# Kernel tuning notes

Measured on AMD Instinct MI355X. Metric: run time of the kernel, lower is better.

Reference implementation:

```python
import jax, jax.numpy as jnp
import numpy as np

DIM = 2048
N_HEADS = 16
KV_LORA = 512
NOPE = 128
ROPE = 64
V_DIM = 128
QK_DIM = NOPE + ROPE  # 192
B, S = 2, 2048
ROPE_THETA = 10000.0
ROPE_FACTOR = 40.0
BETA_FAST, BETA_SLOW = 32, 1
ORIG_LEN, MAX_LEN = 4096, 16384
MSCALE_ARG = 1.0
EPS = 1e-6


def _precompute_freqs(seqlen):
    # DeepSeek YaRN-corrected rotary frequencies (interleaved-pair convention).
    d = ROPE
    freqs = 1.0 / (ROPE_THETA ** (np.arange(0, d, 2, dtype=np.float64) / d))
    if MAX_LEN > ORIG_LEN:
        def corr_dim(n_rot):
            return d * np.log(ORIG_LEN / (n_rot * 2 * np.pi)) / (2 * np.log(ROPE_THETA))
        low = max(int(np.floor(corr_dim(BETA_FAST))), 0)
        high = min(int(np.ceil(corr_dim(BETA_SLOW))), d - 1)
        smooth = 1.0 - np.clip((np.arange(d // 2) - low) / max(high - low, 1e-3), 0, 1)
        freqs = freqs / ROPE_FACTOR * (1 - smooth) + freqs * smooth
    t = np.arange(seqlen, dtype=np.float64)
    ang = np.outer(t, freqs)  # [S, d/2]
    return np.cos(ang).astype(np.float32), np.sin(ang).astype(np.float32)


def softmax_scale():
    scale = QK_DIM ** -0.5
    if MAX_LEN > ORIG_LEN:
        m = 0.1 * MSCALE_ARG * float(np.log(ROPE_FACTOR)) + 1.0
        scale = scale * m * m
    return scale


def setup_inputs() -> dict:
    key = jax.random.key(0)
    ks = jax.random.split(key, 6)
    w_std = 0.02
    fc, fs = _precompute_freqs(S)
    return {
        "x": jax.random.normal(ks[0], (B, S, DIM), jnp.float32),
        "wq": jax.random.normal(ks[1], (N_HEADS * QK_DIM, DIM), jnp.float32) * w_std,
        "wkv_a": jax.random.normal(ks[2], (KV_LORA + ROPE, DIM), jnp.float32) * w_std,
        "kv_norm_w": jnp.ones((KV_LORA,), jnp.float32),
        "wkv_b": jax.random.normal(ks[3], (N_HEADS * (NOPE + V_DIM), KV_LORA), jnp.float32) * w_std,
        "wo": jax.random.normal(ks[4], (DIM, N_HEADS * V_DIM), jnp.float32) * w_std,
        "freqs_cos": jnp.asarray(fc),
        "freqs_sin": jnp.asarray(fs),
    }


def _apply_rotary(x, cos, sin):
    # x: [B, S, H, d]; interleaved complex pairs, cos/sin: [S, d/2]
    xr = x.reshape(*x.shape[:-1], -1, 2)
    x_re, x_im = xr[..., 0], xr[..., 1]
    c = cos[None, :, None, :]
    s = sin[None, :, None, :]
    y_re = x_re * c - x_im * s
    y_im = x_re * s + x_im * c
    return jnp.stack((y_re, y_im), axis=-1).reshape(x.shape)


def _rmsnorm(x, w):
    return x * jax.lax.rsqrt(jnp.mean(x * x, axis=-1, keepdims=True) + EPS) * w


def reference(x, wq, wkv_a, kv_norm_w, wkv_b, wo, freqs_cos, freqs_sin):
    b, s, _ = x.shape
    # Q projection (q_lora_rank == 0 path)
    q = (x @ wq.T).reshape(b, s, N_HEADS, QK_DIM)
    q_nope, q_pe = q[..., :NOPE], q[..., NOPE:]
    q_pe = _apply_rotary(q_pe, freqs_cos, freqs_sin)
    # Low-rank KV compression
    kv = x @ wkv_a.T  # [B, S, 512+64]
    kv_c, k_pe = kv[..., :KV_LORA], kv[..., KV_LORA:]
    k_pe = _apply_rotary(k_pe[:, :, None, :], freqs_cos, freqs_sin)  # [B,S,1,64]
    kv_c = _rmsnorm(kv_c, kv_norm_w)
    kvb = (kv_c @ wkv_b.T).reshape(b, s, N_HEADS, NOPE + V_DIM)
    k_nope, v = kvb[..., :NOPE], kvb[..., NOPE:]
    k = jnp.concatenate([k_nope, jnp.broadcast_to(k_pe, (b, s, N_HEADS, ROPE))], axis=-1)
    # Causal attention
    scores = jnp.einsum("bshd,bthd->bhst", q, k) * softmax_scale()
    causal = jnp.tril(jnp.ones((s, s), bool))
    scores = jnp.where(causal[None, None], scores, jnp.float32(-1e30))
    p = jax.nn.softmax(scores, axis=-1)
    out = jnp.einsum("bhst,bthd->bshd", p, v).reshape(b, s, N_HEADS * V_DIM)
    return out @ wo.T
```

## Files before the change

### kernel.cpp

```cpp
#include <hip/hip_runtime.h>
#include <math.h>

#define NH      16
#define D_NOPE  128
#define D_ROPE  64
#define D_QK    192
#define D_V     128
#define KV_LORA 512
#define NB      2
#define SEQ     2048
#define NTOK    (NB*SEQ)
#define QROW    (NH*D_QK)
#define KVBROW  (NH*(D_NOPE+D_V))
#define EPSF    1e-6f

typedef unsigned short u16;
typedef float  floatx4 __attribute__((ext_vector_type(4)));
typedef __bf16 bf16x8  __attribute__((ext_vector_type(8)));
typedef u16    u16x4   __attribute__((ext_vector_type(4)));
typedef u16    u16x8   __attribute__((ext_vector_type(8)));

__device__ __forceinline__ u16 f2bf(float f) {
    unsigned u = __builtin_bit_cast(unsigned, f);
    return (u16)((u + 0x7fffu + ((u >> 16) & 1u)) >> 16);
}

__device__ __forceinline__ void async_copy16(const void* g, void* l) {
    __builtin_amdgcn_global_load_lds(
        (const __attribute__((address_space(1))) unsigned int*)g,
        (__attribute__((address_space(3))) unsigned int*)l,
        16, 0, 0);
}

__global__ __launch_bounds__(256) void cast_all(const float* __restrict__ x,
                                                const float* __restrict__ wq,
                                                const float* __restrict__ wkva,
                                                const float* __restrict__ wkvb,
                                                const float* __restrict__ wo,
                                                u16* __restrict__ xb,
                                                u16* __restrict__ wqb,
                                                u16* __restrict__ wkvab,
                                                u16* __restrict__ wkvbb,
                                                u16* __restrict__ wob) {
    int blk = blockIdx.x;
    const float* src; u16* dst; bool pad = false;
    if (blk < 8192)        { src = x;    dst = xb; }
    else if (blk < 14336)  { blk -= 8192;  src = wq;   dst = wqb; }
    else if (blk < 15616)  { blk -= 14336; src = wkva; dst = wkvab; pad = true; }
    else if (blk < 17664)  { blk -= 15616; src = wkvb; dst = wkvbb; }
    else                   { blk -= 17664; src = wo;   dst = wob; }
    const int i = (blk * 256 + threadIdx.x) * 4;
    u16x4 o;
    if (pad && (i >> 11) >= 576) {
        o[0] = 0; o[1] = 0; o[2] = 0; o[3] = 0;
    } else {
        const float4 v = *(const float4*)&src[i];
        o[0] = f2bf(v.x); o[1] = f2bf(v.y); o[2] = f2bf(v.z); o[3] = f2bf(v.w);
    }
    *(u16x4*)&dst[i] = o;
}

template<int MODE>
__global__ __launch_bounds__(256) void gemm_mfma(const u16* __restrict__ A,
                                                 const u16* __restrict__ B,
                                                 void* __restrict__ Cout,
                                                 u16* __restrict__ kbuf,
                                                 u16* __restrict__ vT,
                                                 int M, int N, int K) {
    __shared__ u16 As[128 * 32];
    __shared__ u16 Bs[128 * 32];
    const int tid  = threadIdx.x;
    const int wave = tid >> 6, lane = tid & 63;
    const int m0 = blockIdx.y * 128, n0 = blockIdx.x * 128;
    const int wm = (wave & 1) * 64, wn = (wave >> 1) * 64;

    const int srow = wave * 32 + (lane >> 2);
    const int kch  = (lane & 3) * 8;
    const u16* gA0 = A + (size_t)(m0 + srow) * K + kch;
    const u16* gA1 = gA0 + (size_t)16 * K;
    const u16* gB0 = B + (size_t)(n0 + srow) * K + kch;
    const u16* gB1 = gB0 + (size_t)16 * K;
    u16* lA0 = &As[(wave * 32) * 32];
    u16* lA1 = &As[(wave * 32 + 16) * 32];
    u16* lB0 = &Bs[(wave * 32) * 32];
    u16* lB1 = &Bs[(wave * 32 + 16) * 32];

    floatx4 acc[4][4];
#pragma unroll
    for (int i = 0; i < 4; ++i)
#pragma unroll
        for (int j = 0; j < 4; ++j) acc[i][j] = 0.f;

    const int lrow = lane & 15;
    const int lkh  = (lane >> 4) * 8;

    for (int k0 = 0; k0 < K; k0 += 32) {
        __syncthreads();
        async_copy16(gA0 + k0, lA0);
        async_copy16(gA1 + k0, lA1);
        async_copy16(gB0 + k0, lB0);
        async_copy16(gB1 + k0, lB1);
        __syncthreads();
        bf16x8 a[4], b[4];
#pragma unroll
        for (int mi = 0; mi < 4; ++mi)
            a[mi] = *(const bf16x8*)&As[(wm + mi * 16 + lrow) * 32 + lkh];
#pragma unroll
        for (int ni = 0; ni < 4; ++ni)
            b[ni] = *(const bf16x8*)&Bs[(wn + ni * 16 + lrow) * 32 + lkh];
#pragma unroll
        for (int mi = 0; mi < 4; ++mi)
#pragma unroll
            for (int ni = 0; ni < 4; ++ni)
                acc[mi][ni] = __builtin_amdgcn_mfma_f32_16x16x32_bf16(
                    a[mi], b[ni], acc[mi][ni], 0, 0, 0);
    }

    const int crow = (lane >> 4) * 4, ccol = lane & 15;
#pragma unroll
    for (int mi = 0; mi < 4; ++mi)
#pragma unroll
        for (int ni = 0; ni < 4; ++ni) {
            const int m = m0 + wm + mi * 16 + crow;
            const int c = n0 + wn + ni * 16 + ccol;
            if (MODE == 0) {
                float* cp = (float*)Cout + (size_t)m * N + c;
#pragma unroll
                for (int r = 0; r < 4; ++r) cp[(size_t)r * N] = acc[mi][ni][r];
            } else if (MODE == 1) {
                u16* cp = (u16*)Cout + (size_t)m * N + c;
#pragma unroll
                for (int r = 0; r < 4; ++r) cp[(size_t)r * N] = f2bf(acc[mi][ni][r]);
            } else {
                const int hh = c >> 8, j = c & 255;
                const int bb = m >> 11, t = m & 2047;
                if (j < 128) {
#pragma unroll
                    for (int r = 0; r < 4; ++r)
                        kbuf[(((size_t)hh * 2 + bb) * 2048 + t + r) * 192 + j] =
                            f2bf(acc[mi][ni][r]);
                } else {
                    u16x4 pk;
#pragma unroll
                    for (int r = 0; r < 4; ++r) pk[r] = f2bf(acc[mi][ni][r]);
                    *(u16x4*)&vT[(((size_t)hh * 2 + bb) * 128 + (j - 128)) * 2048 + t] = pk;
                }
            }
        }
}


__global__ __launch_bounds__(256) void kv_fix(const float* __restrict__ kv_raw,
                                              const float* __restrict__ w,
                                              const float* __restrict__ fcos,
                                              const float* __restrict__ fsin,
                                              u16* __restrict__ kvn_bf,
                                              u16* __restrict__ kbuf) {
    const int row = blockIdx.x;
    const int tid = threadIdx.x;
    const float* src = kv_raw + (size_t)row * 640;
    const float v0 = src[tid];
    const float v1 = src[256 + tid];
    float ss = v0 * v0 + v1 * v1;
#pragma unroll
    for (int off = 32; off > 0; off >>= 1) ss += __shfl_down(ss, off, 64);
    __shared__ float red[4];
    __shared__ float kpe_s[64];
    if ((tid & 63) == 0) red[tid >> 6] = ss;
    if (tid < 32) {
        const int s = row & (SEQ - 1);
        const float c  = fcos[s * 32 + tid];
        const float sn = fsin[s * 32 + tid];
        const float xr = src[KV_LORA + 2 * tid];
        const float xi = src[KV_LORA + 2 * tid + 1];
        kpe_s[2 * tid]     = xr * c - xi * sn;
        kpe_s[2 * tid + 1] = xr * sn + xi * c;
    }
    __syncthreads();
    const float tot = red[0] + red[1] + red[2] + red[3];
    const float inv = rsqrtf(tot * (1.0f / KV_LORA) + EPSF);
    kvn_bf[(size_t)row * KV_LORA + tid]       = f2bf(v0 * inv * w[tid]);
    kvn_bf[(size_t)row * KV_LORA + 256 + tid] = f2bf(v1 * inv * w[256 + tid]);
    const int bb = row >> 11, t = row & 2047;
    const int hh = tid >> 4, dg = (tid & 15) * 4;
    u16x4 pk;
#pragma unroll
    for (int j = 0; j < 4; ++j) pk[j] = f2bf(kpe_s[dg + j]);
    *(u16x4*)&kbuf[(((size_t)hh * 2 + bb) * 2048 + t) * 192 + 128 + dg] = pk;
}

__global__ __launch_bounds__(256, 2) void attn_mfma(const u16* __restrict__ qbf,
                                                    const u16* __restrict__ kbuf,
                                                    const u16* __restrict__ vT,
                                                    u16* __restrict__ att,
                                                    float scale) {
    __shared__ __attribute__((aligned(16))) u16 Ks[2][6 * 64 * 32];
    __shared__ __attribute__((aligned(16))) u16 Ps[4][32 * 72];
    const int x = blockIdx.x;
    const int qt_base = (x & 1) ? (15 - (x >> 1)) : (x >> 1);
    const int qt = blockIdx.z ? (15 - qt_base) : qt_base;
    const int h = blockIdx.y, b = blockIdx.z;
    const int tid = threadIdx.x, wave = tid >> 6, lane = tid & 63;
    const int l15 = lane & 15, lg = lane >> 4;

    const u16* kb_base = kbuf + ((size_t)(h * 2 + b)) * 2048 * 192;
    const u16* vt_base = vT   + ((size_t)(h * 2 + b)) * 128 * 2048;

    int qrow[2];
    bf16x8 qf[2][6];
#pragma unroll
    for (int g = 0; g < 2; ++g) {
        qrow[g] = qt * 128 + g * 64 + wave * 16 + l15;
        const size_t qoff = ((size_t)(b * SEQ + qrow[g])) * QROW + h * 192 + lg * 8;
#pragma unroll
        for (int s = 0; s < 6; ++s) qf[g][s] = *(const bf16x8*)&qbf[qoff + s * 32];
    }

    floatx4 oacc[2][8];
#pragma unroll
    for (int g = 0; g < 2; ++g)
#pragma unroll
        for (int v = 0; v < 8; ++v) oacc[g][v] = 0.f;
    float m_run[2] = {-1e30f, -1e30f}, l_run[2] = {0.f, 0.f};

    auto stageK = [&](int bufi, int tt) {
#pragma unroll
        for (int i = 0; i < 6; ++i) {
            const int base = (wave * 6 + i) * 64;
            const int slot = base + lane;
            const int s = slot >> 8, r = slot & 255, tk = r >> 2, ch = r & 3;
            async_copy16(kb_base + ((size_t)(tt + tk)) * 192 + s * 32 + ch * 8,
                         &Ks[bufi][base * 8]);
        }
    };

    const int kt_max = 2 * qt + 1;
    stageK(0, 0);
    __syncthreads();

    for (int kt = 0; kt <= kt_max; ++kt) {
        const int t0 = kt * 64;
        const int cur = kt & 1;

        const u16* vrow = vt_base + (size_t)l15 * 2048 + t0 + lg * 8;
        bf16x8 vregA[8], vregB[8];
#pragma unroll
        for (int vt = 0; vt < 8; ++vt)
            vregA[vt] = *(const bf16x8*)&vrow[(size_t)vt * 16 * 2048];

        if (kt < kt_max) stageK(cur ^ 1, t0 + 64);

        floatx4 sacc[2][4];
#pragma unroll
        for (int g = 0; g < 2; ++g)
#pragma unroll
            for (int mt = 0; mt < 4; ++mt) sacc[g][mt] = 0.f;
        __builtin_amdgcn_s_setprio(1);
#pragma unroll
        for (int s = 0; s < 6; ++s) {
#pragma unroll
            for (int mt = 0; mt < 4; ++mt) {
                const bf16x8 kf = *(const bf16x8*)&Ks[cur][(s * 64 + mt * 16 + l15) * 32 + lg * 8];
#pragma unroll
                for (int g = 0; g < 2; ++g)
                    sacc[g][mt] = __builtin_amdgcn_mfma_f32_16x16x32_bf16(
                        kf, qf[g][s], sacc[g][mt], 0, 0, 0);
            }
        }
        __builtin_amdgcn_s_setprio(0);

#pragma unroll
        for (int vt = 0; vt < 8; ++vt)
            vregB[vt] = *(const bf16x8*)&vrow[(size_t)vt * 16 * 2048 + 32];

        float alpha[2];
#pragma unroll
        for (int g = 0; g < 2; ++g) {
            const bool full = (t0 + 63) <= (qt * 128 + g * 64 + wave * 16);
            float p[16];
            float tmax = -1e30f;
#pragma unroll
            for (int mt = 0; mt < 4; ++mt)
#pragma unroll
                for (int r = 0; r < 4; ++r) {
                    float v = sacc[g][mt][r] * scale;
                    if (!full) {
                        const int tglob = t0 + mt * 16 + lg * 4 + r;
                        v = (tglob <= qrow[g]) ? v : -1e30f;
                    }
                    p[mt * 4 + r] = v;
                    tmax = fmaxf(tmax, v);
                }
            tmax = fmaxf(tmax, __shfl_xor(tmax, 16));
            tmax = fmaxf(tmax, __shfl_xor(tmax, 32));
            const float mnew = fmaxf(m_run[g], tmax);
            alpha[g] = __expf(m_run[g] - mnew);
            m_run[g] = mnew;
            float rsum = 0.f;
#pragma unroll
            for (int k = 0; k < 16; ++k) { p[k] = __expf(p[k] - mnew); rsum += p[k]; }
            rsum += __shfl_xor(rsum, 16);
            rsum += __shfl_xor(rsum, 32);
            l_run[g] = l_run[g] * alpha[g] + rsum;
#pragma unroll
            for (int mt = 0; mt < 4; ++mt) {
                u16x4 pk;
#pragma unroll
                for (int r = 0; r < 4; ++r) pk[r] = f2bf(p[mt * 4 + r]);
                *(u16x4*)&Ps[wave][(g * 16 + l15) * 72 + mt * 16 + lg * 4] = pk;
            }
        }
#pragma unroll
        for (int g = 0; g < 2; ++g) {
            float af[4];
#pragma unroll
            for (int r = 0; r < 4; ++r) af[r] = __shfl(alpha[g], lg * 4 + r);
#pragma unroll
            for (int vt = 0; vt < 8; ++vt)
#pragma unroll
                for (int r = 0; r < 4; ++r) oacc[g][vt][r] *= af[r];
        }
        __builtin_amdgcn_s_setprio(1);
#pragma unroll
        for (int s = 0; s < 2; ++s) {
            bf16x8 pf[2];
#pragma unroll
            for (int g = 0; g < 2; ++g)
                pf[g] = *(const bf16x8*)&Ps[wave][(g * 16 + l15) * 72 + s * 32 + lg * 8];
#pragma unroll
            for (int vt = 0; vt < 8; ++vt) {
                const bf16x8 vf = s ? vregB[vt] : vregA[vt];
#pragma unroll
                for (int g = 0; g < 2; ++g)
                    oacc[g][vt] = __builtin_amdgcn_mfma_f32_16x16x32_bf16(
                        pf[g], vf, oacc[g][vt], 0, 0, 0);
            }
        }
        __builtin_amdgcn_s_setprio(0);

        __syncthreads();
    }
#pragma unroll
    for (int g = 0; g < 2; ++g) {
        float lf[4];
#pragma unroll
        for (int r = 0; r < 4; ++r) lf[r] = 1.0f / __shfl(l_run[g], lg * 4 + r);
#pragma unroll
        for (int vt = 0; vt < 8; ++vt)
#pragma unroll
            for (int r = 0; r < 4; ++r) {
                const int orow = b * SEQ + qt * 128 + g * 64 + wave * 16 + lg * 4 + r;
                att[(size_t)orow * 2048 + h * 128 + vt * 16 + l15] =
                    f2bf(oacc[g][vt][r] * lf[r]);
            }
    }
}

extern "C" void kernel_launch(void* const* d_in, const int* in_sizes, int n_in,
                              void* d_out, int out_size, void* d_ws, size_t ws_size,
                              hipStream_t stream) {
    const float* x     = (const float*)d_in[0];
    const float* wq    = (const float*)d_in[1];
    const float* wkv_a = (const float*)d_in[2];
    const float* knw   = (const float*)d_in[3];
    const float* wkv_b = (const float*)d_in[4];
    const float* wo    = (const float*)d_in[5];
    const float* fcos  = (const float*)d_in[6];
    const float* fsin  = (const float*)d_in[7];
    float* out = (float*)d_out;

    char* w = (char*)d_ws;
    u16*   x_bf    = (u16*)w;  w += (size_t)NTOK * 2048 * 2;
    u16*   wq_bf   = (u16*)w;  w += (size_t)QROW * 2048 * 2;
    u16*   wkva_bf = (u16*)w;  w += (size_t)640 * 2048 * 2;
    u16*   wkvb_bf = (u16*)w;  w += (size_t)KVBROW * KV_LORA * 2;
    u16*   wo_bf   = (u16*)w;  w += (size_t)2048 * 2048 * 2;
    u16*   q_bf    = (u16*)w;  w += (size_t)NTOK * QROW * 2;
    float* kv_raw  = (float*)w; w += (size_t)NTOK * 640 * 4;
    u16*   kvn_bf  = (u16*)w;  w += (size_t)NTOK * KV_LORA * 2;
    u16*   kbuf    = (u16*)w;  w += (size_t)NH * NB * SEQ * 192 * 2;
    u16*   vT      = (u16*)w;  w += (size_t)NH * NB * 128 * SEQ * 2;
    u16*   att_bf  = (u16*)w;  w += (size_t)NTOK * 2048 * 2;

    const double mm = 0.1 * 1.0 * log(40.0) + 1.0;
    const float scale = (float)((1.0 / sqrt((double)D_QK)) * mm * mm);

    dim3 blk(256);
    cast_all<<<dim3(21760), blk, 0, stream>>>(x, wq, wkv_a, wkv_b, wo,
                                              x_bf, wq_bf, wkva_bf, wkvb_bf, wo_bf);
    gemm_mfma<1><<<dim3(QROW / 128, NTOK / 128), blk, 0, stream>>>(
        x_bf, wq_bf, q_bf, nullptr, nullptr, NTOK, QROW, 2048);
    gemm_mfma<0><<<dim3(640 / 128, NTOK / 128), blk, 0, stream>>>(
        x_bf, wkva_bf, kv_raw, nullptr, nullptr, NTOK, 640, 2048);
    kv_fix<<<dim3(NTOK), blk, 0, stream>>>(kv_raw, knw, fcos, fsin, kvn_bf, kbuf);
    gemm_mfma<2><<<dim3(KVBROW / 128, NTOK / 128), blk, 0, stream>>>(
        kvn_bf, wkvb_bf, nullptr, kbuf, vT, NTOK, KVBROW, KV_LORA);
    attn_mfma<<<dim3(SEQ / 128, NH, NB), blk, 0, stream>>>(q_bf, kbuf, vT, att_bf, scale);
    gemm_mfma<0><<<dim3(2048 / 128, NTOK / 128), blk, 0, stream>>>(
        att_bf, wo_bf, out, nullptr, nullptr, NTOK, 2048, 2048);
}
```

Baseline: 514.8 us.

## Stage V tiles through LDS and defer softmax rescaling in attention

```diff
diff --git a/kernel.cpp b/kernel.cpp
--- a/kernel.cpp
+++ b/kernel.cpp
@@ -195,7 +195,8 @@
                                                     u16* __restrict__ att,
                                                     float scale) {
     __shared__ __attribute__((aligned(16))) u16 Ks[2][6 * 64 * 32];
-    __shared__ __attribute__((aligned(16))) u16 Ps[4][32 * 72];
+    __shared__ __attribute__((aligned(16))) u16 Vs[2 * 128 * 32];
+    __shared__ __attribute__((aligned(16))) u16 Ps[4][16 * 72];
     const int x = blockIdx.x;
     const int qt_base = (x & 1) ? (15 - (x >> 1)) : (x >> 1);
     const int qt = blockIdx.z ? (15 - qt_base) : qt_base;
@@ -233,6 +234,16 @@
                          &Ks[bufi][base * 8]);
         }
     };
+    auto stageV = [&](int tt) {
+#pragma unroll
+        for (int i = 0; i < 4; ++i) {
+            const int base = (wave * 4 + i) * 64;
+            const int slot = base + lane;
+            const int s = slot >> 9, r = slot & 511, v = r >> 2, ch = r & 3;
+            async_copy16(vt_base + ((size_t)v) * 2048 + tt + s * 32 + ch * 8,
+                         &Vs[base * 8]);
+        }
+    };
 
     const int kt_max = 2 * qt + 1;
     stageK(0, 0);
@@ -242,12 +253,7 @@
         const int t0 = kt * 64;
         const int cur = kt & 1;
 
-        const u16* vrow = vt_base + (size_t)l15 * 2048 + t0 + lg * 8;
-        bf16x8 vregA[8], vregB[8];
-#pragma unroll
-        for (int vt = 0; vt < 8; ++vt)
-            vregA[vt] = *(const bf16x8*)&vrow[(size_t)vt * 16 * 2048];
-
+        stageV(t0);
         if (kt < kt_max) stageK(cur ^ 1, t0 + 64);
 
         floatx4 sacc[2][4];
@@ -269,11 +275,7 @@
         }
         __builtin_amdgcn_s_setprio(0);
 
-#pragma unroll
-        for (int vt = 0; vt < 8; ++vt)
-            vregB[vt] = *(const bf16x8*)&vrow[(size_t)vt * 16 * 2048 + 32];
-
-        float alpha[2];
+        u16x4 pk[2][4];
 #pragma unroll
         for (int g = 0; g < 2; ++g) {
             const bool full = (t0 + 63) <= (qt * 128 + g * 64 + wave * 16);
@@ -293,48 +295,57 @@
                 }
             tmax = fmaxf(tmax, __shfl_xor(tmax, 16));
             tmax = fmaxf(tmax, __shfl_xor(tmax, 32));
-            const float mnew = fmaxf(m_run[g], tmax);
-            alpha[g] = __expf(m_run[g] - mnew);
-            m_run[g] = mnew;
+            const bool defer = __all(tmax <= m_run[g] + 8.0f);
+            float alph = 1.0f;
+            float mnew = m_run[g];
+            if (!defer) {
+                mnew = fmaxf(m_run[g], tmax);
+                alph = __expf(m_run[g] - mnew);
+                m_run[g] = mnew;
+            }
             float rsum = 0.f;
 #pragma unroll
             for (int k = 0; k < 16; ++k) { p[k] = __expf(p[k] - mnew); rsum += p[k]; }
             rsum += __shfl_xor(rsum, 16);
             rsum += __shfl_xor(rsum, 32);
-            l_run[g] = l_run[g] * alpha[g] + rsum;
-#pragma unroll
-            for (int mt = 0; mt < 4; ++mt) {
-                u16x4 pk;
-#pragma unroll
-                for (int r = 0; r < 4; ++r) pk[r] = f2bf(p[mt * 4 + r]);
-                *(u16x4*)&Ps[wave][(g * 16 + l15) * 72 + mt * 16 + lg * 4] = pk;
+            if (!defer) {
+                l_run[g] = l_run[g] * alph + rsum;
+                float af[4];
+#pragma unroll
+                for (int r = 0; r < 4; ++r) af[r] = __shfl(alph, lg * 4 + r);
+#pragma unroll
+                for (int vt = 0; vt < 8; ++vt)
+#pragma unroll
+                    for (int r = 0; r < 4; ++r) oacc[g][vt][r] *= af[r];
+            } else {
+                l_run[g] += rsum;
             }
-        }
+#pragma unroll
+            for (int mt = 0; mt < 4; ++mt)
+#pragma unroll
+                for (int r = 0; r < 4; ++r) pk[g][mt][r] = f2bf(p[mt * 4 + r]);
+        }
+
+        __syncthreads();
+
+        __builtin_amdgcn_s_setprio(1);
 #pragma unroll
         for (int g = 0; g < 2; ++g) {
-            float af[4];
-#pragma unroll
-            for (int r = 0; r < 4; ++r) af[r] = __shfl(alpha[g], lg * 4 + r);
-#pragma unroll
-            for (int vt = 0; vt < 8; ++vt)
-#pragma unroll
-                for (int r = 0; r < 4; ++r) oacc[g][vt][r] *= af[r];
-        }
-        __builtin_amdgcn_s_setprio(1);
-#pragma unroll
-        for (int s = 0; s < 2; ++s) {
+#pragma unroll
+            for (int mt = 0; mt < 4; ++mt)
+                *(u16x4*)&Ps[wave][l15 * 72 + mt * 16 + lg * 4] = pk[g][mt];
             bf16x8 pf[2];
 #pragma unroll
-            for (int g = 0; g < 2; ++g)
-                pf[g] = *(const bf16x8*)&Ps[wave][(g * 16 + l15) * 72 + s * 32 + lg * 8];
-#pragma unroll
-            for (int vt = 0; vt < 8; ++vt) {
-                const bf16x8 vf = s ? vregB[vt] : vregA[vt];
-#pragma unroll
-                for (int g = 0; g < 2; ++g)
+            for (int s = 0; s < 2; ++s)
+                pf[s] = *(const bf16x8*)&Ps[wave][l15 * 72 + s * 32 + lg * 8];
+#pragma unroll
+            for (int s = 0; s < 2; ++s)
+#pragma unroll
+                for (int vt = 0; vt < 8; ++vt) {
+                    const bf16x8 vf = *(const bf16x8*)&Vs[(s * 128 + vt * 16 + l15) * 32 + lg * 8];
                     oacc[g][vt] = __builtin_amdgcn_mfma_f32_16x16x32_bf16(
-                        pf[g], vf, oacc[g][vt], 0, 0, 0);
-            }
+                        pf[s], vf, oacc[g][vt], 0, 0, 0);
+                }
         }
         __builtin_amdgcn_s_setprio(0);
 
```

New measurement: 441.1 us. -14.3%, faster.
